# Optimization experiments

Measured on AMD Instinct MI355X. Metric: run time of the kernel, lower is better.

Reference implementation:

```python
import jax, jax.numpy as jnp
import numpy as np

N_NODES = 100000
N_EDGES = 1600000
N_GRAPHS = 4096
HID = 512
OUT_DIM = 12


def setup_inputs() -> dict:
    key = jax.random.key(0)
    ks = jax.random.split(key, 16)
    x = jax.random.normal(ks[0], (N_NODES, 7), dtype=jnp.float32)
    edge_index = jax.random.randint(ks[1], (2, N_EDGES), 0, N_NODES, dtype=jnp.int32)
    batch = jnp.sort(jax.random.randint(ks[2], (N_NODES,), 0, N_GRAPHS, dtype=jnp.int32))

    def lin(k, i, o):
        s = 1.0 / np.sqrt(i)
        kw, kb = jax.random.split(k)
        return (jax.random.uniform(kw, (i, o), jnp.float32, -s, s),
                jax.random.uniform(kb, (o,), jnp.float32, -s, s))

    c1_w1, c1_b1 = lin(ks[3], 7, HID)
    c1_w2, c1_b2 = lin(ks[4], HID, HID)
    c2_w1, c2_b1 = lin(ks[5], HID, HID)
    c2_w2, c2_b2 = lin(ks[6], HID, HID)
    c3_w1, c3_b1 = lin(ks[7], HID, HID)
    c3_w2, c3_b2 = lin(ks[8], HID, HID)
    lin_w1, lin_b1 = lin(ks[9], HID, 256)
    lin_w2, lin_b2 = lin(ks[10], 256, OUT_DIM)
    return dict(x=x, edge_index=edge_index, batch=batch,
                c1_w1=c1_w1, c1_b1=c1_b1, c1_w2=c1_w2, c1_b2=c1_b2,
                c2_w1=c2_w1, c2_b1=c2_b1, c2_w2=c2_w2, c2_b2=c2_b2,
                c3_w1=c3_w1, c3_b1=c3_b1, c3_w2=c3_w2, c3_b2=c3_b2,
                lin_w1=lin_w1, lin_b1=lin_b1, lin_w2=lin_w2, lin_b2=lin_b2)


def _gin_conv(x, src, dst, w1, b1, w2, b2):
    # GINConv (eps=0): h_i = mlp(x_i + sum_{j in N(i)} x_j)
    agg = jax.ops.segment_sum(x[src], dst, num_segments=N_NODES)
    h = x + agg
    h = jax.nn.relu(h @ w1 + b1) @ w2 + b2
    return h


def reference(x, edge_index, batch,
              c1_w1, c1_b1, c1_w2, c1_b2,
              c2_w1, c2_b1, c2_w2, c2_b2,
              c3_w1, c3_b1, c3_w2, c3_b2,
              lin_w1, lin_b1, lin_w2, lin_b2):
    src, dst = edge_index[0], edge_index[1]
    h = jax.nn.relu(_gin_conv(x, src, dst, c1_w1, c1_b1, c1_w2, c1_b2))
    h = jax.nn.relu(_gin_conv(h, src, dst, c2_w1, c2_b1, c2_w2, c2_b2))
    h = jax.nn.relu(_gin_conv(h, src, dst, c3_w1, c3_b1, c3_w2, c3_b2))
    # global mean pool over graphs in batch
    sums = jax.ops.segment_sum(h, batch, num_segments=N_GRAPHS)
    cnts = jax.ops.segment_sum(jnp.ones((h.shape[0],), h.dtype), batch, num_segments=N_GRAPHS)
    pooled = sums / jnp.maximum(cnts, 1.0)[:, None]
    return jax.nn.relu(pooled @ lin_w1 + lin_b1) @ lin_w2 + lin_b2
```

## Files before the change

kernel.cpp:

```cpp
#include <hip/hip_runtime.h>
#include <hip/hip_bf16.h>
#include <cstddef>
#include <cstdint>

#define N_NODES   100000
#define M_PAD     100096
#define N_EDGES   1600000
#define N_GRAPHS  4096
#define HID       512
#define OUT_DIM   12

typedef unsigned short u16;
typedef __attribute__((ext_vector_type(8))) short bf16x8;
typedef __attribute__((ext_vector_type(4))) float f32x4;

__device__ inline float bf2f(u16 u) {
    union { uint32_t i; float f; } v; v.i = (uint32_t)u << 16; return v.f;
}
__device__ inline u16 f2bf(float f) {
    union { float f; uint32_t i; } v; v.f = f;
    uint32_t r = v.i + 0x7FFFu + ((v.i >> 16) & 1u);
    return (u16)(r >> 16);
}

__device__ inline void load8_bf(const u16* p, float o[8]) {
    uint4 u = *(const uint4*)p;
    uint32_t w[4] = {u.x, u.y, u.z, u.w};
    #pragma unroll
    for (int i = 0; i < 4; ++i) {
        o[2*i]   = bf2f((u16)(w[i] & 0xFFFFu));
        o[2*i+1] = bf2f((u16)(w[i] >> 16));
    }
}
__device__ inline void store8_bf(u16* p, const float o[8]) {
    uint4 u;
    u.x = (uint32_t)f2bf(o[0]) | ((uint32_t)f2bf(o[1]) << 16);
    u.y = (uint32_t)f2bf(o[2]) | ((uint32_t)f2bf(o[3]) << 16);
    u.z = (uint32_t)f2bf(o[4]) | ((uint32_t)f2bf(o[5]) << 16);
    u.w = (uint32_t)f2bf(o[6]) | ((uint32_t)f2bf(o[7]) << 16);
    *(uint4*)p = u;
}
__device__ inline void store8_bf_nt(u16* p, const float o[8]) {
    unsigned long long lo =
        (unsigned long long)((uint32_t)f2bf(o[0]) | ((uint32_t)f2bf(o[1]) << 16)) |
        ((unsigned long long)((uint32_t)f2bf(o[2]) | ((uint32_t)f2bf(o[3]) << 16)) << 32);
    unsigned long long hi =
        (unsigned long long)((uint32_t)f2bf(o[4]) | ((uint32_t)f2bf(o[5]) << 16)) |
        ((unsigned long long)((uint32_t)f2bf(o[6]) | ((uint32_t)f2bf(o[7]) << 16)) << 32);
    __builtin_nontemporal_store(lo, (unsigned long long*)p);
    __builtin_nontemporal_store(hi, (unsigned long long*)(p + 4));
}

__device__ inline void gld16(const void* g, void* l) {
    __builtin_amdgcn_global_load_lds(
        (const __attribute__((address_space(1))) void*)g,
        (__attribute__((address_space(3))) void*)(uint32_t)(uintptr_t)l,
        16, 0, 0);
}

__global__ void zero_ints(int* __restrict__ p, int n) {
    int i = blockIdx.x * blockDim.x + threadIdx.x;
    if (i < n) p[i] = 0;
}

__global__ void hist_kernel(const int* __restrict__ dst, int* __restrict__ counts) {
    int e = blockIdx.x * blockDim.x + threadIdx.x;
    if (e < N_EDGES) atomicAdd(&counts[dst[e]], 1);
}

#define SCAN_NB 98

__global__ __launch_bounds__(1024) void scan_chunks(const int* __restrict__ counts,
                                                    int* __restrict__ row_start,
                                                    int* __restrict__ partials) {
    __shared__ int smem[1024];
    int tid = threadIdx.x;
    int i = blockIdx.x * 1024 + tid;
    int v = (i < N_NODES) ? counts[i] : 0;
    smem[tid] = v;
    __syncthreads();
    for (int off = 1; off < 1024; off <<= 1) {
        int t = (tid >= off) ? smem[tid - off] : 0;
        __syncthreads();
        smem[tid] += t;
        __syncthreads();
    }
    if (i < N_NODES) row_start[i + 1] = smem[tid];
    if (tid == 1023) partials[blockIdx.x] = smem[1023];
}

__global__ void scan_partials(int* __restrict__ partials) {
    if (threadIdx.x == 0 && blockIdx.x == 0) {
        int run = 0;
        for (int b = 0; b < SCAN_NB; ++b) {
            int t = partials[b];
            partials[b] = run;
            run += t;
        }
    }
}

__global__ __launch_bounds__(1024) void scan_add_offsets(int* __restrict__ row_start,
                                                         const int* __restrict__ partials) {
    int i = blockIdx.x * 1024 + threadIdx.x;
    if (i == 0) row_start[0] = 0;
    if (i < N_NODES) row_start[i + 1] += partials[blockIdx.x];
}

__global__ void cursor_init(const int* __restrict__ row_start, int* __restrict__ cursor) {
    int i = blockIdx.x * blockDim.x + threadIdx.x;
    if (i < N_NODES) cursor[i] = row_start[i];
}

__global__ void scatter_edges(const int* __restrict__ src, const int* __restrict__ dst,
                              int* __restrict__ cursor, int* __restrict__ sorted_src) {
    int e = blockIdx.x * blockDim.x + threadIdx.x;
    if (e < N_EDGES) {
        int p = atomicAdd(&cursor[dst[e]], 1);
        p = min(max(p, 0), N_EDGES - 1);
        sorted_src[p] = src[e];
    }
}

__global__ __launch_bounds__(256) void transpose5_to_bf16(const float* __restrict__ W0,
                                                          const float* __restrict__ W1,
                                                          const float* __restrict__ W2,
                                                          const float* __restrict__ W3,
                                                          const float* __restrict__ W4,
                                                          u16* __restrict__ Wt) {
    __shared__ float t[32][33];
    const float* Ws[5] = {W0, W1, W2, W3, W4};
    const float* W = Ws[blockIdx.z];
    u16* dst = Wt + (size_t)blockIdx.z * HID * HID;
    int bx = blockIdx.x * 32, by = blockIdx.y * 32;
    int tx = threadIdx.x & 31, ty = threadIdx.x >> 5;
    #pragma unroll
    for (int i = 0; i < 32; i += 8)
        t[ty + i][tx] = W[(size_t)(by + ty + i) * HID + bx + tx];
    __syncthreads();
    #pragma unroll
    for (int i = 0; i < 32; i += 8)
        dst[(size_t)(bx + ty + i) * HID + by + tx] = f2bf(t[tx][ty + i]);
}

__global__ __launch_bounds__(256) void agg_full(const u16* __restrict__ X,
                                                const int* __restrict__ row_start,
                                                const int* __restrict__ sorted_src,
                                                u16* __restrict__ Out) {
    int node = blockIdx.x * 4 + (threadIdx.x >> 6);
    if (node >= N_NODES) return;
    int lane = threadIdx.x & 63;
    float acc[8];
    load8_bf(X + (size_t)node * HID + lane * 8, acc);
    int e0 = min(row_start[node], N_EDGES);
    int e1 = min(row_start[node + 1], N_EDGES);
    for (int e = e0; e < e1; ++e) {
        unsigned si = min((unsigned)sorted_src[e], (unsigned)(N_NODES - 1));
        float v[8];
        load8_bf(X + (size_t)si * HID + lane * 8, v);
        #pragma unroll
        for (int k = 0; k < 8; ++k) acc[k] += v[k];
    }
    store8_bf_nt(Out + (size_t)node * HID + lane * 8, acc);
}

__global__ __launch_bounds__(64) void agg7_kernel(const float* __restrict__ x,
                                                  const int* __restrict__ row_start,
                                                  const int* __restrict__ sorted_src,
                                                  float* __restrict__ out) {
    int node = blockIdx.x * 8 + (threadIdx.x >> 3);
    int d = threadIdx.x & 7;
    if (node >= N_NODES || d >= 7) return;
    float acc = x[(size_t)node * 7 + d];
    int e0 = min(row_start[node], N_EDGES);
    int e1 = min(row_start[node + 1], N_EDGES);
    for (int e = e0; e < e1; ++e) {
        unsigned si = min((unsigned)sorted_src[e], (unsigned)(N_NODES - 1));
        acc += x[(size_t)si * 7 + d];
    }
    out[(size_t)node * 7 + d] = acc;
}

__global__ __launch_bounds__(256) void gemm_k7_relu(const float* __restrict__ A7,
                                                    const float* __restrict__ W,
                                                    const float* __restrict__ bias,
                                                    u16* __restrict__ C) {
    __shared__ float Wl[7 * HID];
    __shared__ float Bi[HID];
    __shared__ float A7l[128 * 7];
    int tid = threadIdx.x;
    int node0 = blockIdx.x * 128;
    for (int t = tid; t < 7 * HID; t += 256) Wl[t] = W[t];
    for (int t = tid; t < HID; t += 256) Bi[t] = bias[t];
    for (int t = tid; t < 128 * 7; t += 256) {
        int gi = node0 * 7 + t;
        A7l[t] = (gi < N_NODES * 7) ? A7[gi] : 0.f;
    }
    __syncthreads();
    int wid = tid >> 6, lane = tid & 63;
    for (int it = 0; it < 32; ++it) {
        int nl = it * 4 + wid;
        int node = node0 + nl;
        if (node >= N_NODES) break;
        float a[7];
        #pragma unroll
        for (int k = 0; k < 7; ++k) a[k] = A7l[nl * 7 + k];
        float s[8];
        int c0 = lane * 8;
        #pragma unroll
        for (int c = 0; c < 8; ++c) {
            float v = Bi[c0 + c];
            #pragma unroll
            for (int k = 0; k < 7; ++k) v = fmaf(a[k], Wl[k * HID + c0 + c], v);
            s[c] = fmaxf(v, 0.f);
        }
        store8_bf(C + (size_t)node * HID + c0, s);
    }
}

template <bool RELU>
__global__ __launch_bounds__(256) void gemm_mfma_bf16(const u16* __restrict__ A,
                                                      const u16* __restrict__ Wt,
                                                      const float* __restrict__ bias,
                                                      u16* __restrict__ C) {
    __shared__ u16 smem[2 * 2 * 128 * 32];
    u16 (*As)[128][32] = (u16(*)[128][32])smem;
    u16 (*Bs)[128][32] = (u16(*)[128][32])(smem + 2 * 128 * 32);

    const int tid  = threadIdx.x;
    const int wid  = tid >> 6;
    const int lane = tid & 63;
    const int wr = wid >> 1, wc = wid & 1;
    const int row0 = blockIdx.y * 128;
    const int col0 = blockIdx.x * 128;
    const int l15 = lane & 15;
    const int l4  = lane >> 4;

    const int srow = lane >> 2;
    const int scol = (lane & 3) * 8;

    const u16* Ag0 = A  + (size_t)(row0 + wid * 32 + srow) * HID + scol;
    const u16* Bg0 = Wt + (size_t)(col0 + wid * 32 + srow) * HID + scol;

    auto stage = [&](int buf, int k0) {
        #pragma unroll
        for (int i = 0; i < 2; ++i) {
            gld16(Ag0 + (size_t)i * 16 * HID + k0, &As[buf][wid * 32 + i * 16][0]);
            gld16(Bg0 + (size_t)i * 16 * HID + k0, &Bs[buf][wid * 32 + i * 16][0]);
        }
    };

    f32x4 acc[4][4] = {};

    stage(0, 0);
    __syncthreads();

    #pragma unroll 4
    for (int kt = 0; kt < 16; ++kt) {
        int cur = kt & 1;
        if (kt < 15) stage(cur ^ 1, (kt + 1) * 32);
        bf16x8 af[4], bfr[4];
        #pragma unroll
        for (int m = 0; m < 4; ++m)
            af[m] = *(const bf16x8*)&As[cur][wr * 64 + m * 16 + l15][l4 * 8];
        #pragma unroll
        for (int n = 0; n < 4; ++n)
            bfr[n] = *(const bf16x8*)&Bs[cur][wc * 64 + n * 16 + l15][l4 * 8];
        #pragma unroll
        for (int m = 0; m < 4; ++m)
            #pragma unroll
            for (int n = 0; n < 4; ++n)
                acc[m][n] = __builtin_amdgcn_mfma_f32_16x16x32_bf16(af[m], bfr[n],
                                                                    acc[m][n], 0, 0, 0);
        __syncthreads();
    }

    u16* Ct = smem;
    #pragma unroll
    for (int m = 0; m < 4; ++m) {
        #pragma unroll
        for (int n = 0; n < 4; ++n) {
            int col = wc * 64 + n * 16 + l15;
            float b = bias[col0 + col];
            #pragma unroll
            for (int i = 0; i < 4; ++i) {
                int r = wr * 64 + m * 16 + l4 * 4 + i;
                float v = acc[m][n][i] + b;
                if (RELU) v = fmaxf(v, 0.f);
                Ct[r * 128 + col] = f2bf(v);
            }
        }
    }
    __syncthreads();
    #pragma unroll
    for (int j = 0; j < 8; ++j) {
        int c = tid + j * 256;
        int r = c >> 4, cc = (c & 15) * 8;
        uint4 v = *(const uint4*)&Ct[r * 128 + cc];
        *(uint4*)&C[(size_t)(row0 + r) * HID + col0 + cc] = v;
    }
}

template <bool RELU>
__global__ __launch_bounds__(256) void gemm_tiled_f32(const float* __restrict__ A,
                                                      const float* __restrict__ W,
                                                      const float* __restrict__ bias,
                                                      float* __restrict__ C,
                                                      int M, int N, int K) {
    __shared__ float As[16][68];
    __shared__ float Bs[16][68];
    int tid = threadIdx.x;
    int tx = tid & 15, ty = tid >> 4;
    int col0 = blockIdx.x * 64;
    int row0 = blockIdx.y * 64;
    float acc[4][4] = {};

    for (int k0 = 0; k0 < K; k0 += 16) {
        {
            int r = tid >> 2, c = (tid & 3) * 4;
            float4 v = make_float4(0.f, 0.f, 0.f, 0.f);
            int gr = row0 + r;
            if (gr < M) v = *reinterpret_cast<const float4*>(A + (size_t)gr * K + k0 + c);
            As[c + 0][r] = v.x; As[c + 1][r] = v.y; As[c + 2][r] = v.z; As[c + 3][r] = v.w;
        }
        {
            int r = tid >> 4, c = (tid & 15) * 4;
            int gc = col0 + c;
            float4 v = make_float4(0.f, 0.f, 0.f, 0.f);
            const float* wp = W + (size_t)(k0 + r) * N + gc;
            if (gc + 3 < N) {
                v = *reinterpret_cast<const float4*>(wp);
            } else {
                float t0 = (gc + 0 < N) ? wp[0] : 0.f;
                float t1 = (gc + 1 < N) ? wp[1] : 0.f;
                float t2 = (gc + 2 < N) ? wp[2] : 0.f;
                v = make_float4(t0, t1, t2, 0.f);
            }
            *reinterpret_cast<float4*>(&Bs[r][c]) = v;
        }
        __syncthreads();
        #pragma unroll
        for (int k = 0; k < 16; ++k) {
            float a[4], b[4];
            *(float4*)a = *(const float4*)&As[k][ty * 4];
            *(float4*)b = *(const float4*)&Bs[k][tx * 4];
            #pragma unroll
            for (int i = 0; i < 4; ++i)
                #pragma unroll
                for (int j = 0; j < 4; ++j)
                    acc[i][j] = fmaf(a[i], b[j], acc[i][j]);
        }
        __syncthreads();
    }

    #pragma unroll
    for (int i = 0; i < 4; ++i) {
        int r = row0 + ty * 4 + i;
        if (r >= M) break;
        #pragma unroll
        for (int j = 0; j < 4; ++j) {
            int cidx = col0 + tx * 4 + j;
            if (cidx >= N) continue;
            float v = acc[i][j] + bias[cidx];
            if (RELU) v = fmaxf(v, 0.f);
            C[(size_t)r * N + cidx] = v;
        }
    }
}

__global__ void graph_bounds(const int* __restrict__ batch, int* __restrict__ g_start) {
    int g = blockIdx.x * blockDim.x + threadIdx.x;
    if (g > N_GRAPHS) return;
    int lo = 0, hi = N_NODES;
    while (lo < hi) {
        int mid = (lo + hi) >> 1;
        if (batch[mid] < g) lo = mid + 1; else hi = mid;
    }
    g_start[g] = lo;
}

__global__ __launch_bounds__(256) void pool_kernel(const u16* __restrict__ H,
                                                   const int* __restrict__ g_start,
                                                   float* __restrict__ pooled) {
    int g = blockIdx.x * 4 + (threadIdx.x >> 6);
    if (g >= N_GRAPHS) return;
    int lane = threadIdx.x & 63;
    int s = g_start[g], e = g_start[g + 1];
    float acc[8] = {};
    for (int n = s; n < e; ++n) {
        float v[8];
        load8_bf(H + (size_t)n * HID + lane * 8, v);
        #pragma unroll
        for (int k = 0; k < 8; ++k) acc[k] += v[k];
    }
    float inv = 1.f / fmaxf((float)(e - s), 1.f);
    float* o = pooled + (size_t)g * HID + lane * 8;
    #pragma unroll
    for (int k = 0; k < 8; ++k) o[k] = acc[k] * inv;
}

__global__ void diag_kernel(float* __restrict__ out, int n, float v) {
    int i = blockIdx.x * blockDim.x + threadIdx.x;
    if (i < n) out[i] = v;
}

static inline size_t rnd256(size_t b) { return (b + 255) & ~(size_t)255; }

extern "C" void kernel_launch(void* const* d_in, const int* in_sizes, int n_in,
                              void* d_out, int out_size, void* d_ws, size_t ws_size,
                              hipStream_t stream) {
    (void)in_sizes; (void)n_in;
    const float* x     = (const float*)d_in[0];
    const int*   ei    = (const int*)d_in[1];
    const int*   batch = (const int*)d_in[2];
    const int* src = ei;
    const int* dst = ei + N_EDGES;

    const float* c1_w1 = (const float*)d_in[3];
    const float* c1_b1 = (const float*)d_in[4];
    const float* c1_w2 = (const float*)d_in[5];
    const float* c1_b2 = (const float*)d_in[6];
    const float* c2_w1 = (const float*)d_in[7];
    const float* c2_b1 = (const float*)d_in[8];
    const float* c2_w2 = (const float*)d_in[9];
    const float* c2_b2 = (const float*)d_in[10];
    const float* c3_w1 = (const float*)d_in[11];
    const float* c3_b1 = (const float*)d_in[12];
    const float* c3_w2 = (const float*)d_in[13];
    const float* c3_b2 = (const float*)d_in[14];
    const float* lin_w1 = (const float*)d_in[15];
    const float* lin_b1 = (const float*)d_in[16];
    const float* lin_w2 = (const float*)d_in[17];
    const float* lin_b2 = (const float*)d_in[18];
    float* out = (float*)d_out;

    size_t off = 0;
    auto alloc = [&](size_t bytes) -> void* {
        void* p = (char*)d_ws + off;
        off += rnd256(bytes);
        return p;
    };
    u16*   b0        = (u16*)alloc((size_t)M_PAD * HID * 2);
    u16*   b1        = (u16*)alloc((size_t)M_PAD * HID * 2);
    float* agg7buf   = (float*)alloc((size_t)N_NODES * 7 * 4);
    int*   counts    = (int*)alloc((size_t)N_NODES * 4);
    int*   cursor    = (int*)alloc((size_t)N_NODES * 4);
    int*   row_start = (int*)alloc((size_t)(N_NODES + 1) * 4);
    int*   sorted_src= (int*)alloc((size_t)N_EDGES * 4);
    int*   g_start   = (int*)alloc((size_t)(N_GRAPHS + 1) * 4);
    int*   partials  = (int*)alloc((size_t)SCAN_NB * 4);
    float* pooled    = (float*)alloc((size_t)N_GRAPHS * HID * 4);
    char*  hh_slot   = (char*)alloc((size_t)N_GRAPHS * 256 * 4);
    float* hh        = (float*)hh_slot;
    u16*   wt        = (u16*)hh_slot;
    u16* c1w2T = wt + 0 * HID * HID;
    u16* c2w1T = wt + 1 * HID * HID;
    u16* c2w2T = wt + 2 * HID * HID;
    u16* c3w1T = wt + 3 * HID * HID;
    u16* c3w2T = wt + 4 * HID * HID;

    if (off > ws_size) {
        diag_kernel<<<(out_size + 255) / 256, 256, 0, stream>>>(
            out, out_size, (float)(ws_size >> 20));
        return;
    }

    zero_ints<<<(N_NODES + 255) / 256, 256, 0, stream>>>(counts, N_NODES);
    hist_kernel<<<(N_EDGES + 255) / 256, 256, 0, stream>>>(dst, counts);
    scan_chunks<<<SCAN_NB, 1024, 0, stream>>>(counts, row_start, partials);
    scan_partials<<<1, 64, 0, stream>>>(partials);
    scan_add_offsets<<<SCAN_NB, 1024, 0, stream>>>(row_start, partials);
    cursor_init<<<(N_NODES + 255) / 256, 256, 0, stream>>>(row_start, cursor);
    scatter_edges<<<(N_EDGES + 255) / 256, 256, 0, stream>>>(src, dst, cursor, sorted_src);
    graph_bounds<<<(N_GRAPHS + 256) / 256, 256, 0, stream>>>(batch, g_start);
    transpose5_to_bf16<<<dim3(HID / 32, HID / 32, 5), 256, 0, stream>>>(
        c1_w2, c2_w1, c2_w2, c3_w1, c3_w2, wt);

    dim3 mgrid(HID / 128, M_PAD / 128);
    const int aggGrid = N_NODES / 4;

    agg7_kernel<<<(N_NODES + 7) / 8, 64, 0, stream>>>(x, row_start, sorted_src, agg7buf);
    gemm_k7_relu<<<(N_NODES + 127) / 128, 256, 0, stream>>>(agg7buf, c1_w1, c1_b1, b0);
    gemm_mfma_bf16<true><<<mgrid, 256, 0, stream>>>(b0, c1w2T, c1_b2, b1);
    agg_full<<<aggGrid, 256, 0, stream>>>(b1, row_start, sorted_src, b0);
    gemm_mfma_bf16<true><<<mgrid, 256, 0, stream>>>(b0, c2w1T, c2_b1, b1);
    gemm_mfma_bf16<true><<<mgrid, 256, 0, stream>>>(b1, c2w2T, c2_b2, b0);
    agg_full<<<aggGrid, 256, 0, stream>>>(b0, row_start, sorted_src, b1);
    gemm_mfma_bf16<true><<<mgrid, 256, 0, stream>>>(b1, c3w1T, c3_b1, b0);
    gemm_mfma_bf16<true><<<mgrid, 256, 0, stream>>>(b0, c3w2T, c3_b2, b1);
    pool_kernel<<<N_GRAPHS / 4, 256, 0, stream>>>(b1, g_start, pooled);
    gemm_tiled_f32<true><<<dim3(256 / 64, N_GRAPHS / 64), 256, 0, stream>>>(
        pooled, lin_w1, lin_b1, hh, N_GRAPHS, 256, HID);
    gemm_tiled_f32<false><<<dim3(1, N_GRAPHS / 64), 256, 0, stream>>>(
        hh, lin_w2, lin_b2, out, N_GRAPHS, OUT_DIM, 256);
}
```

Measured before the change: 1.448 ms.

## Load GEMM weight fragments directly from global and swizzle block order

The bf16 MFMA GEMM no longer stages the weight tile in shared memory. Each lane now reads its B fragments straight from global memory, which is L2-resident, and only the A tile is double-buffered in LDS. Blocks are also remapped to a 1D grid that groups 8 row tiles by 4 column tiles, so consecutive blocks share A rows for better cache locality. This removes LDS traffic and half the staging work, at the cost of global-load latency in the inner loop that the kernel does not prefetch.

```diff
diff --git a/kernel.cpp b/kernel.cpp
--- a/kernel.cpp
+++ b/kernel.cpp
@@ -218,54 +218,77 @@
     }
 }
 
+#define NROWT (M_PAD / 128)
+
 template <bool RELU>
 __global__ __launch_bounds__(256) void gemm_mfma_bf16(const u16* __restrict__ A,
                                                       const u16* __restrict__ Wt,
                                                       const float* __restrict__ bias,
                                                       u16* __restrict__ C) {
-    __shared__ u16 smem[2 * 2 * 128 * 32];
+    __shared__ u16 smem[128 * 128];
     u16 (*As)[128][32] = (u16(*)[128][32])smem;
-    u16 (*Bs)[128][32] = (u16(*)[128][32])(smem + 2 * 128 * 32);
+
+    int bid = blockIdx.x;
+    int row, col;
+    {
+        int g = bid >> 5;
+        if (g < NROWT / 8) {
+            int w = bid & 31;
+            row = g * 8 + (w & 7);
+            col = w >> 3;
+        } else {
+            int w = bid - (NROWT / 8) * 32;
+            int rem = NROWT - (NROWT / 8) * 8;
+            row = (NROWT / 8) * 8 + w % rem;
+            col = w / rem;
+        }
+    }
+    const int row0 = row * 128;
+    const int col0 = col * 128;
 
     const int tid  = threadIdx.x;
     const int wid  = tid >> 6;
     const int lane = tid & 63;
     const int wr = wid >> 1, wc = wid & 1;
-    const int row0 = blockIdx.y * 128;
-    const int col0 = blockIdx.x * 128;
     const int l15 = lane & 15;
     const int l4  = lane >> 4;
 
     const int srow = lane >> 2;
     const int scol = (lane & 3) * 8;
 
-    const u16* Ag0 = A  + (size_t)(row0 + wid * 32 + srow) * HID + scol;
-    const u16* Bg0 = Wt + (size_t)(col0 + wid * 32 + srow) * HID + scol;
-
-    auto stage = [&](int buf, int k0) {
-        #pragma unroll
-        for (int i = 0; i < 2; ++i) {
+    const u16* Ag0 = A + (size_t)(row0 + wid * 32 + srow) * HID + scol;
+    auto stageA = [&](int buf, int k0) {
+        #pragma unroll
+        for (int i = 0; i < 2; ++i)
             gld16(Ag0 + (size_t)i * 16 * HID + k0, &As[buf][wid * 32 + i * 16][0]);
-            gld16(Bg0 + (size_t)i * 16 * HID + k0, &Bs[buf][wid * 32 + i * 16][0]);
-        }
     };
 
+    const u16* Bp[4];
+    #pragma unroll
+    for (int n = 0; n < 4; ++n)
+        Bp[n] = Wt + (size_t)(col0 + wc * 64 + n * 16 + l15) * HID + l4 * 8;
+
+    float bcol[4];
+    #pragma unroll
+    for (int n = 0; n < 4; ++n) bcol[n] = bias[col0 + wc * 64 + n * 16 + l15];
+
     f32x4 acc[4][4] = {};
 
-    stage(0, 0);
+    stageA(0, 0);
     __syncthreads();
 
     #pragma unroll 4
     for (int kt = 0; kt < 16; ++kt) {
         int cur = kt & 1;
-        if (kt < 15) stage(cur ^ 1, (kt + 1) * 32);
-        bf16x8 af[4], bfr[4];
+        if (kt < 15) stageA(cur ^ 1, (kt + 1) * 32);
+        bf16x8 bfr[4];
+        #pragma unroll
+        for (int n = 0; n < 4; ++n)
+            bfr[n] = *(const bf16x8*)(Bp[n] + kt * 32);
+        bf16x8 af[4];
         #pragma unroll
         for (int m = 0; m < 4; ++m)
             af[m] = *(const bf16x8*)&As[cur][wr * 64 + m * 16 + l15][l4 * 8];
-        #pragma unroll
-        for (int n = 0; n < 4; ++n)
-            bfr[n] = *(const bf16x8*)&Bs[cur][wc * 64 + n * 16 + l15][l4 * 8];
         #pragma unroll
         for (int m = 0; m < 4; ++m)
             #pragma unroll
@@ -280,14 +303,13 @@
     for (int m = 0; m < 4; ++m) {
         #pragma unroll
         for (int n = 0; n < 4; ++n) {
-            int col = wc * 64 + n * 16 + l15;
-            float b = bias[col0 + col];
+            int c = wc * 64 + n * 16 + l15;
             #pragma unroll
             for (int i = 0; i < 4; ++i) {
                 int r = wr * 64 + m * 16 + l4 * 4 + i;
-                float v = acc[m][n][i] + b;
+                float v = acc[m][n][i] + bcol[n];
                 if (RELU) v = fmaxf(v, 0.f);
-                Ct[r * 128 + col] = f2bf(v);
+                Ct[r * 128 + c] = f2bf(v);
             }
         }
     }
@@ -476,7 +498,7 @@
     transpose5_to_bf16<<<dim3(HID / 32, HID / 32, 5), 256, 0, stream>>>(
         c1_w2, c2_w1, c2_w2, c3_w1, c3_w2, wt);
 
-    dim3 mgrid(HID / 128, M_PAD / 128);
+    const int mgrid = NROWT * 4;
     const int aggGrid = N_NODES / 4;
 
     agg7_kernel<<<(N_NODES + 7) / 8, 64, 0, stream>>>(x, row_start, sorted_src, agg7buf);
```

After: 1.619 ms. +11.8%, slower.

## Replace 128x128 tiled MFMA GEMM with full-width row-block GEMM

Applied to the files above, without the earlier changes.

The double-buffered 128x128 LDS-tiled bf16 MFMA GEMM is replaced by a kernel where each block owns 32 rows and all 512 output columns. The A tile is staged into padded LDS once, and the weight operand is read straight from global memory (expected to stay in L2) each k-step. This removes the per-k-step barriers and B staging, and writes full rows of output. The cost is that every block re-reads the whole 512x512 weight matrix, so total L2 traffic rises, and global-load latency for B is exposed with no prefetch.

```diff
diff --git a/kernel.cpp b/kernel.cpp
--- a/kernel.cpp
+++ b/kernel.cpp
@@ -218,86 +218,77 @@
     }
 }
 
+#define LDW 520
+
 template <bool RELU>
-__global__ __launch_bounds__(256) void gemm_mfma_bf16(const u16* __restrict__ A,
-                                                      const u16* __restrict__ Wt,
-                                                      const float* __restrict__ bias,
-                                                      u16* __restrict__ C) {
-    __shared__ u16 smem[2 * 2 * 128 * 32];
-    u16 (*As)[128][32] = (u16(*)[128][32])smem;
-    u16 (*Bs)[128][32] = (u16(*)[128][32])(smem + 2 * 128 * 32);
-
+__global__ __launch_bounds__(256) void gemm_fullw(const u16* __restrict__ A,
+                                                  const u16* __restrict__ Wt,
+                                                  const float* __restrict__ bias,
+                                                  u16* __restrict__ C) {
+    __shared__ u16 As[32][LDW];
     const int tid  = threadIdx.x;
     const int wid  = tid >> 6;
     const int lane = tid & 63;
-    const int wr = wid >> 1, wc = wid & 1;
-    const int row0 = blockIdx.y * 128;
-    const int col0 = blockIdx.x * 128;
     const int l15 = lane & 15;
     const int l4  = lane >> 4;
-
-    const int srow = lane >> 2;
-    const int scol = (lane & 3) * 8;
-
-    const u16* Ag0 = A  + (size_t)(row0 + wid * 32 + srow) * HID + scol;
-    const u16* Bg0 = Wt + (size_t)(col0 + wid * 32 + srow) * HID + scol;
-
-    auto stage = [&](int buf, int k0) {
-        #pragma unroll
-        for (int i = 0; i < 2; ++i) {
-            gld16(Ag0 + (size_t)i * 16 * HID + k0, &As[buf][wid * 32 + i * 16][0]);
-            gld16(Bg0 + (size_t)i * 16 * HID + k0, &Bs[buf][wid * 32 + i * 16][0]);
-        }
-    };
-
-    f32x4 acc[4][4] = {};
-
-    stage(0, 0);
-    __syncthreads();
+    const int row0 = blockIdx.x * 32;
+
+    #pragma unroll
+    for (int r = 0; r < 8; ++r) {
+        int row = wid * 8 + r;
+        gld16(A + (size_t)(row0 + row) * HID + lane * 8, &As[row][0]);
+    }
+    __syncthreads();
+
+    const u16* Bp[8];
+    float bcol[8];
+    #pragma unroll
+    for (int n = 0; n < 8; ++n) {
+        int col = wid * 128 + n * 16 + l15;
+        Bp[n]  = Wt + (size_t)col * HID + l4 * 8;
+        bcol[n] = bias[col];
+    }
+
+    f32x4 acc[2][8] = {};
 
     #pragma unroll 4
     for (int kt = 0; kt < 16; ++kt) {
-        int cur = kt & 1;
-        if (kt < 15) stage(cur ^ 1, (kt + 1) * 32);
-        bf16x8 af[4], bfr[4];
-        #pragma unroll
-        for (int m = 0; m < 4; ++m)
-            af[m] = *(const bf16x8*)&As[cur][wr * 64 + m * 16 + l15][l4 * 8];
-        #pragma unroll
-        for (int n = 0; n < 4; ++n)
-            bfr[n] = *(const bf16x8*)&Bs[cur][wc * 64 + n * 16 + l15][l4 * 8];
-        #pragma unroll
-        for (int m = 0; m < 4; ++m)
+        bf16x8 bfr[8];
+        #pragma unroll
+        for (int n = 0; n < 8; ++n)
+            bfr[n] = *(const bf16x8*)(Bp[n] + kt * 32);
+        bf16x8 af[2];
+        #pragma unroll
+        for (int m = 0; m < 2; ++m)
+            af[m] = *(const bf16x8*)&As[m * 16 + l15][kt * 32 + l4 * 8];
+        #pragma unroll
+        for (int m = 0; m < 2; ++m)
             #pragma unroll
-            for (int n = 0; n < 4; ++n)
+            for (int n = 0; n < 8; ++n)
                 acc[m][n] = __builtin_amdgcn_mfma_f32_16x16x32_bf16(af[m], bfr[n],
                                                                     acc[m][n], 0, 0, 0);
-        __syncthreads();
-    }
-
-    u16* Ct = smem;
-    #pragma unroll
-    for (int m = 0; m < 4; ++m) {
-        #pragma unroll
-        for (int n = 0; n < 4; ++n) {
-            int col = wc * 64 + n * 16 + l15;
-            float b = bias[col0 + col];
+    }
+
+    __syncthreads();
+    #pragma unroll
+    for (int m = 0; m < 2; ++m)
+        #pragma unroll
+        for (int n = 0; n < 8; ++n) {
+            int c = wid * 128 + n * 16 + l15;
             #pragma unroll
             for (int i = 0; i < 4; ++i) {
-                int r = wr * 64 + m * 16 + l4 * 4 + i;
-                float v = acc[m][n][i] + b;
+                float v = acc[m][n][i] + bcol[n];
                 if (RELU) v = fmaxf(v, 0.f);
-                Ct[r * 128 + col] = f2bf(v);
+                As[m * 16 + l4 * 4 + i][c] = f2bf(v);
             }
         }
-    }
     __syncthreads();
     #pragma unroll
     for (int j = 0; j < 8; ++j) {
         int c = tid + j * 256;
-        int r = c >> 4, cc = (c & 15) * 8;
-        uint4 v = *(const uint4*)&Ct[r * 128 + cc];
-        *(uint4*)&C[(size_t)(row0 + r) * HID + col0 + cc] = v;
+        int r = c >> 6, cc = (c & 63) * 8;
+        uint4 v = *(const uint4*)&As[r][cc];
+        *(uint4*)&C[(size_t)(row0 + r) * HID + cc] = v;
     }
 }
 
@@ -476,18 +467,18 @@
     transpose5_to_bf16<<<dim3(HID / 32, HID / 32, 5), 256, 0, stream>>>(
         c1_w2, c2_w1, c2_w2, c3_w1, c3_w2, wt);
 
-    dim3 mgrid(HID / 128, M_PAD / 128);
+    const int mgrid = M_PAD / 32;
     const int aggGrid = N_NODES / 4;
 
     agg7_kernel<<<(N_NODES + 7) / 8, 64, 0, stream>>>(x, row_start, sorted_src, agg7buf);
     gemm_k7_relu<<<(N_NODES + 127) / 128, 256, 0, stream>>>(agg7buf, c1_w1, c1_b1, b0);
-    gemm_mfma_bf16<true><<<mgrid, 256, 0, stream>>>(b0, c1w2T, c1_b2, b1);
+    gemm_fullw<true><<<mgrid, 256, 0, stream>>>(b0, c1w2T, c1_b2, b1);
     agg_full<<<aggGrid, 256, 0, stream>>>(b1, row_start, sorted_src, b0);
-    gemm_mfma_bf16<true><<<mgrid, 256, 0, stream>>>(b0, c2w1T, c2_b1, b1);
-    gemm_mfma_bf16<true><<<mgrid, 256, 0, stream>>>(b1, c2w2T, c2_b2, b0);
+    gemm_fullw<true><<<mgrid, 256, 0, stream>>>(b0, c2w1T, c2_b1, b1);
+    gemm_fullw<true><<<mgrid, 256, 0, stream>>>(b1, c2w2T, c2_b2, b0);
     agg_full<<<aggGrid, 256, 0, stream>>>(b0, row_start, sorted_src, b1);
-    gemm_mfma_bf16<true><<<mgrid, 256, 0, stream>>>(b1, c3w1T, c3_b1, b0);
-    gemm_mfma_bf16<true><<<mgrid, 256, 0, stream>>>(b0, c3w2T, c3_b2, b1);
+    gemm_fullw<true><<<mgrid, 256, 0, stream>>>(b1, c3w1T, c3_b1, b0);
+    gemm_fullw<true><<<mgrid, 256, 0, stream>>>(b0, c3w2T, c3_b2, b1);
     pool_kernel<<<N_GRAPHS / 4, 256, 0, stream>>>(b1, g_start, pooled);
     gemm_tiled_f32<true><<<dim3(256 / 64, N_GRAPHS / 64), 256, 0, stream>>>(
         pooled, lin_w1, lin_b1, hh, N_GRAPHS, 256, HID);
```

Measured after the change: 1.917 ms. 1.32x slower.

## Unroll gather aggregation by four and pipeline GEMM loads with partial vmcnt waits

Applied to the files above, without the earlier changes.

The aggregation kernel now issues four independent neighbor-row loads per iteration, exposing more memory-level parallelism to hide gather latency. The GEMM main loop is fully unrolled and replaces __syncthreads with explicit s_waitcnt vmcnt(4) plus raw barriers, so the next tile's global-to-LDS loads stay in flight while the current tile is computed. Scheduling barriers fix the order of LDS reads and MFMAs. The hand-written waitcnt counts depend on the exact number of loads per stage, which is fragile and could cause races if the stage load count changes.

```diff
diff --git a/kernel.cpp b/kernel.cpp
--- a/kernel.cpp
+++ b/kernel.cpp
@@ -150,18 +150,35 @@
     int node = blockIdx.x * 4 + (threadIdx.x >> 6);
     if (node >= N_NODES) return;
     int lane = threadIdx.x & 63;
+    const size_t coff = (size_t)lane * 8;
     float acc[8];
-    load8_bf(X + (size_t)node * HID + lane * 8, acc);
+    load8_bf(X + (size_t)node * HID + coff, acc);
     int e0 = min(row_start[node], N_EDGES);
     int e1 = min(row_start[node + 1], N_EDGES);
-    for (int e = e0; e < e1; ++e) {
+    int e  = e0;
+    int e4 = e0 + ((e1 - e0) & ~3);
+    for (; e < e4; e += 4) {
+        unsigned s0 = min((unsigned)sorted_src[e + 0], (unsigned)(N_NODES - 1));
+        unsigned s1 = min((unsigned)sorted_src[e + 1], (unsigned)(N_NODES - 1));
+        unsigned s2 = min((unsigned)sorted_src[e + 2], (unsigned)(N_NODES - 1));
+        unsigned s3 = min((unsigned)sorted_src[e + 3], (unsigned)(N_NODES - 1));
+        float v0[8], v1[8], v2[8], v3[8];
+        load8_bf(X + (size_t)s0 * HID + coff, v0);
+        load8_bf(X + (size_t)s1 * HID + coff, v1);
+        load8_bf(X + (size_t)s2 * HID + coff, v2);
+        load8_bf(X + (size_t)s3 * HID + coff, v3);
+        #pragma unroll
+        for (int k = 0; k < 8; ++k)
+            acc[k] += (v0[k] + v1[k]) + (v2[k] + v3[k]);
+    }
+    for (; e < e1; ++e) {
         unsigned si = min((unsigned)sorted_src[e], (unsigned)(N_NODES - 1));
         float v[8];
-        load8_bf(X + (size_t)si * HID + lane * 8, v);
+        load8_bf(X + (size_t)si * HID + coff, v);
         #pragma unroll
         for (int k = 0; k < 8; ++k) acc[k] += v[k];
     }
-    store8_bf_nt(Out + (size_t)node * HID + lane * 8, acc);
+    store8_bf_nt(Out + (size_t)node * HID + coff, acc);
 }
 
 __global__ __launch_bounds__(64) void agg7_kernel(const float* __restrict__ x,
@@ -253,12 +270,19 @@
     f32x4 acc[4][4] = {};
 
     stage(0, 0);
-    __syncthreads();
-
-    #pragma unroll 4
+
+    #pragma unroll
     for (int kt = 0; kt < 16; ++kt) {
-        int cur = kt & 1;
-        if (kt < 15) stage(cur ^ 1, (kt + 1) * 32);
+        const int cur = kt & 1;
+        if (kt < 15) {
+            stage(cur ^ 1, (kt + 1) * 32);
+            asm volatile("s_waitcnt vmcnt(4)" ::: "memory");
+        } else {
+            asm volatile("s_waitcnt vmcnt(0)" ::: "memory");
+        }
+        __builtin_amdgcn_s_barrier();
+        __builtin_amdgcn_sched_barrier(0);
+
         bf16x8 af[4], bfr[4];
         #pragma unroll
         for (int m = 0; m < 4; ++m)
@@ -266,13 +290,16 @@
         #pragma unroll
         for (int n = 0; n < 4; ++n)
             bfr[n] = *(const bf16x8*)&Bs[cur][wc * 64 + n * 16 + l15][l4 * 8];
+        asm volatile("s_waitcnt lgkmcnt(0)" ::: "memory");
+        __builtin_amdgcn_sched_barrier(0);
+
         #pragma unroll
         for (int m = 0; m < 4; ++m)
             #pragma unroll
             for (int n = 0; n < 4; ++n)
                 acc[m][n] = __builtin_amdgcn_mfma_f32_16x16x32_bf16(af[m], bfr[n],
                                                                     acc[m][n], 0, 0, 0);
-        __syncthreads();
+        __builtin_amdgcn_s_barrier();
     }
 
     u16* Ct = smem;
```

New measurement: 1.372 ms. 5.2% less time.
